# Performance work log

Measured on AMD Instinct MI355X. Metric: run time of the kernel, lower is better.

Reference implementation:

```python
import jax, jax.numpy as jnp
import numpy as np

N_NEW = 100000  # number of atoms placed beyond the initial 3 seed coordinates


def setup_inputs() -> dict:
    key = jax.random.key(0)
    k1, k2, k3, k4 = jax.random.split(key, 4)
    # realistic internal coordinates: bond lengths ~1.2-1.6 A, bond angles ~1.5-2.1 rad
    dis = 1.2 + 0.4 * jax.random.uniform(k1, (N_NEW,), dtype=jnp.float32)
    angle = 1.5 + 0.6 * jax.random.uniform(k2, (N_NEW,), dtype=jnp.float32)
    dhd = 2.0 * jnp.pi * jax.random.uniform(k3, (N_NEW,), dtype=jnp.float32) - jnp.pi
    xyz0 = jax.random.normal(k4, (3, 3), dtype=jnp.float32)  # seed atoms c[0..2]
    return {"dis": dis, "angle": angle, "dhd": dhd, "xyz0": xyz0}


def _nerf_chain(xyz0, tt):
    """Sequential NeRF extension: place atom k from atoms k-3,k-2,k-1 and local coords tt[k]."""
    def step(carry, t):
        a, b, c = carry  # c[k-3], c[k-2], c[k-1], each shape [3]
        mk = c - b
        mk_1 = b - a
        mk_n = mk / jnp.sqrt(jnp.sum(mk * mk))
        nk = jnp.cross(mk_1, mk_n)
        nk_n = nk / jnp.sqrt(jnp.sum(nk * nk))
        nk_mk_n = jnp.cross(nk_n, mk_n)
        # R rows = (mk_n, nk_mk_n, nk_n); new = R^T @ t + c
        new = t[0] * mk_n + t[1] * nk_mk_n + t[2] * nk_n + c
        return (b, c, new), new

    _, placed = jax.lax.scan(step, (xyz0[0], xyz0[1], xyz0[2]), tt)
    return jnp.concatenate([xyz0, placed], axis=0)  # [N_NEW+3, 3]


def reference(dis, angle, dhd, xyz0):
    sin_a = jnp.sin(angle)
    t1 = dis * jnp.cos(angle)
    t2 = dis * jnp.cos(dhd) * sin_a
    t3 = dis * jnp.sin(dhd) * sin_a
    tt = jnp.stack([t1, t2, t3], axis=1)  # [N_NEW, 3] local spherical coords
    return _nerf_chain(xyz0, tt)
```

## Files before the change

### kernel.cpp

```cpp
#include <hip/hip_runtime.h>
#include <math.h>


#define BLOCK 256
#define CPT 8

struct AffF { float v[12]; };

__device__ __forceinline__ AffF aff_id() {
    AffF a;
    a.v[0]=1.f; a.v[1]=0.f; a.v[2]=0.f;
    a.v[3]=0.f; a.v[4]=1.f; a.v[5]=0.f;
    a.v[6]=0.f; a.v[7]=0.f; a.v[8]=1.f;
    a.v[9]=0.f; a.v[10]=0.f; a.v[11]=0.f;
    return a;
}

__device__ __forceinline__ AffF aff_compose(const AffF& A, const AffF& B) {
    AffF C;
#pragma unroll
    for (int i = 0; i < 3; i++) {
#pragma unroll
        for (int j = 0; j < 3; j++) {
            C.v[i*3+j] = A.v[i*3+0]*B.v[0+j] + A.v[i*3+1]*B.v[3+j] + A.v[i*3+2]*B.v[6+j];
        }
        C.v[9+i] = A.v[i*3+0]*B.v[9] + A.v[i*3+1]*B.v[10] + A.v[i*3+2]*B.v[11] + A.v[9+i];
    }
    return C;
}

__device__ __forceinline__ AffF make_M(float L, float a, float d) {
    float sa, ca, sd, cd;
    sincosf(a, &sa, &ca);
    sincosf(d, &sd, &cd);
    AffF M;
    M.v[0] = ca;      M.v[1] = -sa;     M.v[2] = 0.f;
    M.v[3] = cd * sa; M.v[4] = cd * ca; M.v[5] = -sd;
    M.v[6] = sd * sa; M.v[7] = sd * ca; M.v[8] = cd;
    M.v[9] = L * ca;  M.v[10] = L * cd * sa; M.v[11] = L * sd * sa;
    return M;
}

__device__ __forceinline__ void lds_store(float (&s)[12][BLOCK], int i, const AffF& a) {
#pragma unroll
    for (int c = 0; c < 12; c++) s[c][i] = a.v[c];
}
__device__ __forceinline__ AffF lds_load(float (&s)[12][BLOCK], int i) {
    AffF a;
#pragma unroll
    for (int c = 0; c < 12; c++) a.v[c] = s[c][i];
    return a;
}

__device__ __forceinline__ void block_scan(float (&s)[12][BLOCK], int tid,
                                           int nvalid, AffF& mine) {
#pragma unroll
    for (int off = 1; off < BLOCK; off <<= 1) {
        bool h = (tid >= off) && (tid < nvalid);
        AffF other;
        if (h) other = lds_load(s, tid - off);
        __syncthreads();
        if (h) {
            mine = aff_compose(other, mine);
            lds_store(s, tid, mine);
        }
        __syncthreads();
    }
}

__global__ __launch_bounds__(BLOCK) void nerf_scan(const float* __restrict__ dis,
                                                   const float* __restrict__ ang,
                                                   const float* __restrict__ dhd,
                                                   const float* __restrict__ xyz0,
                                                   float* __restrict__ out, int n,
                                                   AffF* __restrict__ agg,
                                                   int* __restrict__ flag) {
    __shared__ float s[12][BLOCK];
    __shared__ AffF sBase;
    const int tid = threadIdx.x;
    const int b = blockIdx.x;
    const long base = (long)b * BLOCK * CPT + (long)tid * CPT;

    AffF acc = aff_id();
    float px[CPT][3];
    for (int j = 0; j < CPT; j++) {
        long k = base + j;
        if (k < n) acc = aff_compose(acc, make_M(dis[k], ang[k], dhd[k]));
        px[j][0] = acc.v[9]; px[j][1] = acc.v[10]; px[j][2] = acc.v[11];
    }

    lds_store(s, tid, acc);
    __syncthreads();
    AffF mine = acc;
    block_scan(s, tid, BLOCK, mine);

    AffF excl;
    if (tid > 0) excl = lds_load(s, tid - 1);

    if (tid == BLOCK - 1) {
        float* g = (float*)&agg[b];
#pragma unroll
        for (int c = 0; c < 12; c++) g[c] = mine.v[c];
        __threadfence();
        __hip_atomic_store(&flag[b], b + 1, __ATOMIC_RELEASE, __HIP_MEMORY_SCOPE_AGENT);
    }
    __syncthreads();

    AffF g = aff_id();
    if (tid < b) {
        while (__hip_atomic_load(&flag[tid], __ATOMIC_ACQUIRE, __HIP_MEMORY_SCOPE_AGENT)
               != tid + 1) {
            __builtin_amdgcn_s_sleep(2);
        }
        const float* gp = (const float*)&agg[tid];
#pragma unroll
        for (int c = 0; c < 12; c++) g.v[c] = gp[c];
        lds_store(s, tid, g);
    }
    __syncthreads();
    block_scan(s, tid, b, g);

    if (tid == 0) {
        float ax = xyz0[0], ay = xyz0[1], az = xyz0[2];
        float bx = xyz0[3], by = xyz0[4], bz = xyz0[5];
        float cx = xyz0[6], cy = xyz0[7], cz = xyz0[8];
        float mx = cx - bx, my = cy - by, mz = cz - bz;
        float inv = 1.f / sqrtf(mx*mx + my*my + mz*mz);
        float mnx = mx*inv, mny = my*inv, mnz = mz*inv;
        float ux = bx - ax, uy = by - ay, uz = bz - az;
        float nx = uy*mnz - uz*mny, ny = uz*mnx - ux*mnz, nz = ux*mny - uy*mnx;
        float inv2 = 1.f / sqrtf(nx*nx + ny*ny + nz*nz);
        float nnx = nx*inv2, nny = ny*inv2, nnz = nz*inv2;
        float wx = nny*mnz - nnz*mny, wy = nnz*mnx - nnx*mnz, wz = nnx*mny - nny*mnx;
        AffF F0;
        F0.v[0] = mnx; F0.v[1] = wx; F0.v[2] = nnx;
        F0.v[3] = mny; F0.v[4] = wy; F0.v[5] = nny;
        F0.v[6] = mnz; F0.v[7] = wz; F0.v[8] = nnz;
        F0.v[9] = cx;  F0.v[10] = cy; F0.v[11] = cz;
        sBase = (b == 0) ? F0 : aff_compose(F0, lds_load(s, b - 1));
    }
    if (b == 0 && tid < 9) out[tid] = xyz0[tid];
    __syncthreads();

    AffF E = (tid > 0) ? aff_compose(sBase, excl) : sBase;
    for (int j = 0; j < CPT; j++) {
        long k = base + j;
        if (k < n) {
            float x = E.v[0]*px[j][0] + E.v[1]*px[j][1] + E.v[2]*px[j][2] + E.v[9];
            float y = E.v[3]*px[j][0] + E.v[4]*px[j][1] + E.v[5]*px[j][2] + E.v[10];
            float z = E.v[6]*px[j][0] + E.v[7]*px[j][1] + E.v[8]*px[j][2] + E.v[11];
            long o = (k + 3) * 3;
            out[o + 0] = x; out[o + 1] = y; out[o + 2] = z;
        }
    }
}

extern "C" void kernel_launch(void* const* d_in, const int* in_sizes, int n_in,
                              void* d_out, int out_size, void* d_ws, size_t ws_size,
                              hipStream_t stream) {
    const float* dis  = (const float*)d_in[0];
    const float* ang  = (const float*)d_in[1];
    const float* dhd  = (const float*)d_in[2];
    const float* xyz0 = (const float*)d_in[3];
    float* out = (float*)d_out;
    int n = in_sizes[0];

    AffF* agg = (AffF*)d_ws;
    int* flag = (int*)((char*)d_ws + 16384);
    int nb = (n + BLOCK * CPT - 1) / (BLOCK * CPT);

    nerf_scan<<<nb, BLOCK, 0, stream>>>(dis, ang, dhd, xyz0, out, n, agg, flag);
}
```

Before: 75.34 us.

## Replace LDS block scans with wavefront shuffle scans and stage inputs via LDS

Swaps the shared-memory Hillis-Steele block scan, which needs two barriers per step, for a 64-lane shuffle scan inside each wavefront followed by a short serial combine of the per-wave totals. The lookback across blocks is now done by a single wavefront using shuffles, since there are at most 49 blocks. Inputs are loaded into LDS with coalesced float4 loads and then read per thread as float4 instead of strided scalar global loads. This cuts barrier count and LDS traffic, at the cost of extra shuffle instructions and more LDS use per block.

```diff
diff --git a/kernel.cpp b/kernel.cpp
--- a/kernel.cpp
+++ b/kernel.cpp
@@ -4,6 +4,7 @@
 
 #define BLOCK 256
 #define CPT 8
+#define NELEM (BLOCK * CPT)
 
 struct AffF { float v[12]; };
 
@@ -41,31 +42,11 @@
     return M;
 }
 
-__device__ __forceinline__ void lds_store(float (&s)[12][BLOCK], int i, const AffF& a) {
-#pragma unroll
-    for (int c = 0; c < 12; c++) s[c][i] = a.v[c];
-}
-__device__ __forceinline__ AffF lds_load(float (&s)[12][BLOCK], int i) {
-    AffF a;
-#pragma unroll
-    for (int c = 0; c < 12; c++) a.v[c] = s[c][i];
-    return a;
-}
-
-__device__ __forceinline__ void block_scan(float (&s)[12][BLOCK], int tid,
-                                           int nvalid, AffF& mine) {
-#pragma unroll
-    for (int off = 1; off < BLOCK; off <<= 1) {
-        bool h = (tid >= off) && (tid < nvalid);
-        AffF other;
-        if (h) other = lds_load(s, tid - off);
-        __syncthreads();
-        if (h) {
-            mine = aff_compose(other, mine);
-            lds_store(s, tid, mine);
-        }
-        __syncthreads();
-    }
+__device__ __forceinline__ AffF shfl_up_aff(const AffF& a, int delta) {
+    AffF r;
+#pragma unroll
+    for (int c = 0; c < 12; c++) r.v[c] = __shfl_up(a.v[c], delta, 64);
+    return r;
 }
 
 __global__ __launch_bounds__(BLOCK) void nerf_scan(const float* __restrict__ dis,
@@ -75,52 +56,109 @@
                                                    float* __restrict__ out, int n,
                                                    AffF* __restrict__ agg,
                                                    int* __restrict__ flag) {
-    __shared__ float s[12][BLOCK];
+    __shared__ float sDis[NELEM], sAng[NELEM], sDhd[NELEM];
+    __shared__ float sWave[12][BLOCK / 64];
     __shared__ AffF sBase;
-    const int tid = threadIdx.x;
-    const int b = blockIdx.x;
-    const long base = (long)b * BLOCK * CPT + (long)tid * CPT;
-
-    AffF acc = aff_id();
+
+    const int tid  = threadIdx.x;
+    const int lane = tid & 63;
+    const int w    = tid >> 6;
+    const int b    = blockIdx.x;
+    const int eb   = b * NELEM;
+    const int nblk = min(NELEM, n - eb);
+
+    {
+        int nv4 = nblk >> 2;
+        const float4* gD = (const float4*)(dis + eb);
+        const float4* gA = (const float4*)(ang + eb);
+        const float4* gH = (const float4*)(dhd + eb);
+        float4* lD = (float4*)sDis; float4* lA = (float4*)sAng; float4* lH = (float4*)sDhd;
+        for (int i = tid; i < nv4; i += BLOCK) { lD[i] = gD[i]; lA[i] = gA[i]; lH[i] = gH[i]; }
+        for (int i = (nv4 << 2) + tid; i < nblk; i += BLOCK) {
+            sDis[i] = dis[eb+i]; sAng[i] = ang[eb+i]; sDhd[i] = dhd[eb+i];
+        }
+    }
+    __syncthreads();
+
+    const int lb = tid * CPT;
+    const int nv = max(0, min(CPT, nblk - lb));
+    float ld[CPT], la[CPT], lh[CPT];
+    {
+        const float4* D4 = (const float4*)sDis;
+        const float4* A4 = (const float4*)sAng;
+        const float4* H4 = (const float4*)sDhd;
+        *(float4*)&ld[0] = D4[tid*2]; *(float4*)&ld[4] = D4[tid*2+1];
+        *(float4*)&la[0] = A4[tid*2]; *(float4*)&la[4] = A4[tid*2+1];
+        *(float4*)&lh[0] = H4[tid*2]; *(float4*)&lh[4] = H4[tid*2+1];
+    }
+    AffF acc = (nv > 0) ? make_M(ld[0], la[0], lh[0]) : aff_id();
     float px[CPT][3];
-    for (int j = 0; j < CPT; j++) {
-        long k = base + j;
-        if (k < n) acc = aff_compose(acc, make_M(dis[k], ang[k], dhd[k]));
+    px[0][0] = acc.v[9]; px[0][1] = acc.v[10]; px[0][2] = acc.v[11];
+#pragma unroll
+    for (int j = 1; j < CPT; j++) {
+        if (j < nv) acc = aff_compose(acc, make_M(ld[j], la[j], lh[j]));
         px[j][0] = acc.v[9]; px[j][1] = acc.v[10]; px[j][2] = acc.v[11];
     }
 
-    lds_store(s, tid, acc);
+    AffF mine = acc;
+#pragma unroll
+    for (int off = 1; off < 64; off <<= 1) {
+        AffF other = shfl_up_aff(mine, off);
+        if (lane >= off) mine = aff_compose(other, mine);
+    }
+    if (lane == 63) {
+#pragma unroll
+        for (int c = 0; c < 12; c++) sWave[c][w] = mine.v[c];
+    }
     __syncthreads();
-    AffF mine = acc;
-    block_scan(s, tid, BLOCK, mine);
-
-    AffF excl;
-    if (tid > 0) excl = lds_load(s, tid - 1);
+
+    AffF wpre;
+    if (w > 0) {
+#pragma unroll
+        for (int c = 0; c < 12; c++) wpre.v[c] = sWave[c][0];
+        for (int w2 = 1; w2 < w; w2++) {
+            AffF t;
+#pragma unroll
+            for (int c = 0; c < 12; c++) t.v[c] = sWave[c][w2];
+            wpre = aff_compose(wpre, t);
+        }
+    }
 
     if (tid == BLOCK - 1) {
+        AffF tot = aff_compose(wpre, mine);
         float* g = (float*)&agg[b];
 #pragma unroll
-        for (int c = 0; c < 12; c++) g[c] = mine.v[c];
+        for (int c = 0; c < 12; c++) g[c] = tot.v[c];
         __threadfence();
         __hip_atomic_store(&flag[b], b + 1, __ATOMIC_RELEASE, __HIP_MEMORY_SCOPE_AGENT);
     }
-    __syncthreads();
-
-    AffF g = aff_id();
-    if (tid < b) {
-        while (__hip_atomic_load(&flag[tid], __ATOMIC_ACQUIRE, __HIP_MEMORY_SCOPE_AGENT)
-               != tid + 1) {
-            __builtin_amdgcn_s_sleep(2);
-        }
-        const float* gp = (const float*)&agg[tid];
-#pragma unroll
-        for (int c = 0; c < 12; c++) g.v[c] = gp[c];
-        lds_store(s, tid, g);
-    }
-    __syncthreads();
-    block_scan(s, tid, b, g);
-
-    if (tid == 0) {
+
+    AffF exw = shfl_up_aff(mine, 1);
+    AffF excl;
+    if (lane == 0) { if (w > 0) excl = wpre; }
+    else excl = (w > 0) ? aff_compose(wpre, exw) : exw;
+
+    if (w == 0) {
+        AffF g = aff_id();
+        if (lane < b) {
+            while (__hip_atomic_load(&flag[lane], __ATOMIC_ACQUIRE,
+                                     __HIP_MEMORY_SCOPE_AGENT) != lane + 1) {
+                __builtin_amdgcn_s_sleep(2);
+            }
+            const float* gp = (const float*)&agg[lane];
+#pragma unroll
+            for (int c = 0; c < 12; c++) g.v[c] = gp[c];
+        }
+#pragma unroll
+        for (int off = 1; off < 64; off <<= 1) {
+            AffF other = shfl_up_aff(g, off);
+            if (lane >= off) g = aff_compose(other, g);
+        }
+        AffF tot;
+        if (b > 0) {
+#pragma unroll
+            for (int c = 0; c < 12; c++) tot.v[c] = __shfl(g.v[c], b - 1, 64);
+        }
         float ax = xyz0[0], ay = xyz0[1], az = xyz0[2];
         float bx = xyz0[3], by = xyz0[4], bz = xyz0[5];
         float cx = xyz0[6], cy = xyz0[7], cz = xyz0[8];
@@ -137,15 +175,17 @@
         F0.v[3] = mny; F0.v[4] = wy; F0.v[5] = nny;
         F0.v[6] = mnz; F0.v[7] = wz; F0.v[8] = nnz;
         F0.v[9] = cx;  F0.v[10] = cy; F0.v[11] = cz;
-        sBase = (b == 0) ? F0 : aff_compose(F0, lds_load(s, b - 1));
+        AffF baseT = (b == 0) ? F0 : aff_compose(F0, tot);
+        if (lane == 0) sBase = baseT;
     }
     if (b == 0 && tid < 9) out[tid] = xyz0[tid];
     __syncthreads();
 
-    AffF E = (tid > 0) ? aff_compose(sBase, excl) : sBase;
+    AffF E = (tid == 0) ? sBase : aff_compose(sBase, excl);
+#pragma unroll
     for (int j = 0; j < CPT; j++) {
-        long k = base + j;
-        if (k < n) {
+        if (j < nv) {
+            long k = (long)eb + lb + j;
             float x = E.v[0]*px[j][0] + E.v[1]*px[j][1] + E.v[2]*px[j][2] + E.v[9];
             float y = E.v[3]*px[j][0] + E.v[4]*px[j][1] + E.v[5]*px[j][2] + E.v[10];
             float z = E.v[6]*px[j][0] + E.v[7]*px[j][1] + E.v[8]*px[j][2] + E.v[11];
@@ -167,7 +207,7 @@
 
     AffF* agg = (AffF*)d_ws;
     int* flag = (int*)((char*)d_ws + 16384);
-    int nb = (n + BLOCK * CPT - 1) / (BLOCK * CPT);
+    int nb = (n + NELEM - 1) / NELEM;
 
     nerf_scan<<<nb, BLOCK, 0, stream>>>(dis, ang, dhd, xyz0, out, n, agg, flag);
 }
```

Result: faster. 71.89 us (-4.6%).
